# Optimization experiments

Hardware: AMD Instinct MI355X
Metric: run time of the kernel (lower is better)

The kernel has to match this reference:

```python
import jax, jax.numpy as jnp
import numpy as np

EMBED = 2048
HEADS = 16


def setup_inputs() -> dict:
    key = jax.random.key(0)
    ks = jax.random.split(key, 9)
    N, L, E = 4, 2048, EMBED
    inp = {
        "query": jax.random.normal(ks[0], (N, L, E), dtype=jnp.float32),
        "keys": jax.random.normal(ks[1], (N, L, E), dtype=jnp.float32),
        "values": jax.random.normal(ks[2], (N, L, E), dtype=jnp.float32),
        "mask": jax.random.randint(ks[3], (N, L), 0, 2, dtype=jnp.int32),
        # nn.Linear weights, stored torch-style as (out_features, in_features)
        "Wq": jax.random.normal(ks[4], (E, E), dtype=jnp.float32) * (E ** -0.5),
        "Wk": jax.random.normal(ks[5], (E, E), dtype=jnp.float32) * (E ** -0.5),
        "Wv": jax.random.normal(ks[6], (E, E), dtype=jnp.float32) * (E ** -0.5),
        "Wo": jax.random.normal(ks[7], (E, E), dtype=jnp.float32) * (E ** -0.5),
        "bo": jax.random.normal(ks[8], (E,), dtype=jnp.float32) * 0.01,
    }
    return inp


def reference(query, keys, values, mask, Wq, Wk, Wv, Wo, bo):
    N, Lq, E = query.shape
    Lk = keys.shape[1]
    H = HEADS
    D = E // H
    # projections (torch Linear: y = x @ W.T)
    q = (query @ Wq.T).reshape(N, Lq, H, D)   # nqhd
    k = (keys @ Wk.T).reshape(N, Lk, H, D)    # nkhd
    v = (values @ Wv.T).reshape(N, Lk, H, D)  # nkhd
    # attention scores per head: (N, H, Lq, Lk)
    energy = jnp.einsum('nqhd,nkhd->nhqk', q, k)
    # 2D mask (N, Lk): 0 = masked out, broadcast over heads and query positions
    m = mask[:, None, None, :]
    energy = jnp.where(m == 0, jnp.float32(-1e20), energy)
    # source scales by sqrt(embed_size), not sqrt(head_dim)
    attn = jax.nn.softmax(energy * (E ** -0.5), axis=-1)
    out = jnp.einsum('nhqk,nkhd->nqhd', attn, v).reshape(N, Lq, E)
    return out @ Wo.T + bo
```

## Files before the change

kernel.cpp:

```cpp
#include <hip/hip_runtime.h>
#include <stdint.h>


typedef __bf16 bf16;
typedef __bf16 bf16x2 __attribute__((ext_vector_type(2)));
typedef __bf16 bf16x4 __attribute__((ext_vector_type(4)));
typedef __bf16 bf16x8 __attribute__((ext_vector_type(8)));
typedef float  f32x4  __attribute__((ext_vector_type(4)));
typedef uint32_t u32x4 __attribute__((ext_vector_type(4)));

#define MFMA16(a, b, c) __builtin_amdgcn_mfma_f32_16x16x32_bf16(a, b, c, 0, 0, 0)

__device__ __forceinline__ void gload_lds16(const void* g, void* s) {
  __builtin_amdgcn_global_load_lds(
      (const __attribute__((address_space(1))) void*)g,
      (__attribute__((address_space(3))) void*)s, 16, 0, 0);
}

__device__ __forceinline__ uint32_t pkbf(float a, float b) {
  return __builtin_bit_cast(uint32_t, (bf16x2){(bf16)a, (bf16)b});
}

__device__ __forceinline__ float fexp2(float x) {
  return __builtin_amdgcn_exp2f(x);
}

__global__ __launch_bounds__(256) void cvt8_bf16(const float* __restrict__ s0,
                                                 const float* __restrict__ s1,
                                                 const float* __restrict__ s2,
                                                 const float* __restrict__ s3,
                                                 const float* __restrict__ q,
                                                 bf16* __restrict__ d0,
                                                 bf16* __restrict__ d1,
                                                 bf16* __restrict__ d2,
                                                 bf16* __restrict__ d3,
                                                 bf16* __restrict__ dq,
                                                 long EE) {
  int y = blockIdx.y;
  const float* src;
  bf16* dst;
  if (y < 4) {
    src = y == 0 ? s0 : y == 1 ? s1 : y == 2 ? s2 : s3;
    dst = y == 0 ? d0 : y == 1 ? d1 : y == 2 ? d2 : d3;
  } else {
    src = q + (long)(y - 4) * EE;
    dst = dq + (long)(y - 4) * EE;
  }
  long i = ((long)blockIdx.x * 256 + threadIdx.x) * 4;
  f32x4 f = *(const f32x4*)(src + i);
  bf16x4 h = { (bf16)f.x, (bf16)f.y, (bf16)f.z, (bf16)f.w };
  *(bf16x4*)(dst + i) = h;
}

__global__ __launch_bounds__(256) void gather2_cvt(const float* __restrict__ ks,
                                                   const float* __restrict__ vs,
                                                   bf16* __restrict__ kd,
                                                   bf16* __restrict__ vd,
                                                   const int* __restrict__ idx,
                                                   const int* __restrict__ cnts) {
  long i = (long)blockIdx.x * 256 + threadIdx.x;
  int row = (int)(i >> 8);
  int u = (int)(i & 255);
  int n = row >> 11, p = row & 2047;
  if (p >= cnts[4 + n]) return;
  long srow = ((long)n << 11) + idx[(n << 11) + p];
  long so = srow * 2048 + u * 8;
  long dof = (long)row * 2048 + u * 8;
  {
    f32x4 a = *(const f32x4*)(ks + so);
    f32x4 b = *(const f32x4*)(ks + so + 4);
    bf16x8 h = { (bf16)a.x, (bf16)a.y, (bf16)a.z, (bf16)a.w,
                 (bf16)b.x, (bf16)b.y, (bf16)b.z, (bf16)b.w };
    *(bf16x8*)(kd + dof) = h;
  }
  {
    f32x4 a = *(const f32x4*)(vs + so);
    f32x4 b = *(const f32x4*)(vs + so + 4);
    bf16x8 h = { (bf16)a.x, (bf16)a.y, (bf16)a.z, (bf16)a.w,
                 (bf16)b.x, (bf16)b.y, (bf16)b.z, (bf16)b.w };
    *(bf16x8*)(vd + dof) = h;
  }
}

__global__ __launch_bounds__(256) void mask_compact(const int* __restrict__ mask,
                                                    int* __restrict__ idx,
                                                    int* __restrict__ cnts) {
  const int n = blockIdx.x;
  const int t = threadIdx.x, l = t & 63, w = t >> 6;
  const int* m = mask + n * 2048;
  __shared__ int wtot[4];
  int f[8], tt = 0;
  const int base = t * 8;
#pragma unroll
  for (int i = 0; i < 8; ++i) { f[i] = (m[base + i] != 0); tt += f[i]; }
  int sc = tt;
#pragma unroll
  for (int d = 1; d < 64; d <<= 1) {
    int v = __shfl_up(sc, d);
    if (l >= d) sc += v;
  }
  if (l == 63) wtot[w] = sc;
  __syncthreads();
  int woff = 0;
#pragma unroll
  for (int i = 0; i < 4; ++i) if (i < w) woff += wtot[i];
  int off = woff + sc - tt;
#pragma unroll
  for (int i = 0; i < 8; ++i)
    if (f[i]) { idx[n * 2048 + off] = base + i; ++off; }
  int total = wtot[0] + wtot[1] + wtot[2] + wtot[3];
  for (int p = total + t; p < 2048; p += 256) idx[n * 2048 + p] = 2047;
  if (t == 0) { cnts[n] = total; cnts[4 + n] = (total + 127) & ~127; }
}

template <int QKV, int OUT_F32, int ADD_BIAS>
__global__ __launch_bounds__(512, 2) void gemm256(const bf16* __restrict__ A0,
                                                  const bf16* __restrict__ A1,
                                                  const bf16* __restrict__ A2,
                                                  const bf16* __restrict__ B0,
                                                  const bf16* __restrict__ B1,
                                                  const bf16* __restrict__ B2,
                                                  void* __restrict__ C0,
                                                  void* __restrict__ C1,
                                                  void* __restrict__ C2,
                                                  const float* __restrict__ bias,
                                                  const int* __restrict__ cnts) {
  constexpr int K = 2048, LDC = 2048, NT = 32;
  constexpr int TILE = 256 * 64;
  __shared__ bf16 S[2 * 2 * TILE];
  const int t = threadIdx.x;
  const int l = t & 63, w = t >> 6;
  const int wr = w >> 2, wc = w & 3;
  const int l15 = l & 15, l4 = l >> 4;

  const int z = blockIdx.z;
  const bf16* A = z == 0 ? A0 : z == 1 ? A1 : A2;
  const bf16* B = z == 0 ? B0 : z == 1 ? B1 : B2;
  void* Cout = z == 0 ? C0 : z == 1 ? C1 : C2;

  const int Mb = ((blockIdx.x & 7) << 2) + (blockIdx.x >> 3);
  const long tm = (long)Mb * 256;
  const long tn = (long)blockIdx.y * 256;

  if constexpr (QKV) {
    if (z) {
      int n = (int)(tm >> 11);
      if ((int)(tm & 2047) >= cnts[4 + n]) return;
    }
  }

  const bf16* Ab = A + tm * K;
  const bf16* Bb = B + tn * K;

  auto stage = [&](int T, int p) {
    bf16* sA = S + p * 2 * TILE;
    bf16* sB = sA + TILE;
    const bf16* Ak = Ab + T * 64;
    const bf16* Bk = Bb + T * 64;
#pragma unroll
    for (int i = 0; i < 4; ++i) {
      int u = i * 512 + t;
      int row = u >> 3, slot = u & 7;
      int ss = slot ^ (row & 7);
      gload_lds16(Ak + (long)row * K + ss * 8, sA + u * 8);
    }
#pragma unroll
    for (int i = 0; i < 4; ++i) {
      int u = i * 512 + t;
      int row = u >> 3, slot = u & 7;
      int ss = slot ^ (row & 7);
      gload_lds16(Bk + (long)row * K + ss * 8, sB + u * 8);
    }
  };

  f32x4 acc[8][4];
#pragma unroll
  for (int i = 0; i < 8; ++i)
#pragma unroll
    for (int j = 0; j < 4; ++j) acc[i][j] = (f32x4){0.f, 0.f, 0.f, 0.f};

  stage(0, 0);

  for (int T = 0; T < NT; ++T) {
    const int p = T & 1;
    const bf16* sA = S + p * 2 * TILE;
    const bf16* sB = sA + TILE;

    if (T + 1 < NT) {
      stage(T + 1, p ^ 1);
      asm volatile("s_waitcnt vmcnt(8)" ::: "memory");
    } else {
      asm volatile("s_waitcnt vmcnt(0)" ::: "memory");
    }
    __builtin_amdgcn_s_barrier();
    asm volatile("" ::: "memory");

#pragma unroll
    for (int kk = 0; kk < 2; ++kk) {
      bf16x8 bfr[4];
#pragma unroll
      for (int ni = 0; ni < 4; ++ni) {
        int row = wc * 64 + ni * 16 + l15;
        int slot = (kk * 4 + l4) ^ (row & 7);
        bfr[ni] = *(const bf16x8*)(sB + row * 64 + slot * 8);
      }
#pragma unroll
      for (int mh = 0; mh < 2; ++mh) {
        bf16x8 af[4];
#pragma unroll
        for (int i = 0; i < 4; ++i) {
          int row = wr * 128 + (mh * 4 + i) * 16 + l15;
          int slot = (kk * 4 + l4) ^ (row & 7);
          af[i] = *(const bf16x8*)(sA + row * 64 + slot * 8);
        }
        asm volatile("" ::: "memory");
        __builtin_amdgcn_s_barrier();
        asm volatile("" ::: "memory");
        __builtin_amdgcn_s_setprio(1);
#pragma unroll
        for (int i = 0; i < 4; ++i)
#pragma unroll
          for (int ni = 0; ni < 4; ++ni)
            acc[mh * 4 + i][ni] = MFMA16(af[i], bfr[ni], acc[mh * 4 + i][ni]);
        __builtin_amdgcn_s_setprio(0);
        asm volatile("" ::: "memory");
        __builtin_amdgcn_s_barrier();
        asm volatile("" ::: "memory");
      }
    }
  }

  const float sc = (QKV && blockIdx.z == 0) ? 0.031879357f : 1.0f;
#pragma unroll
  for (int mi = 0; mi < 8; ++mi) {
#pragma unroll
    for (int ni = 0; ni < 4; ++ni) {
      long col = tn + wc * 64 + ni * 16 + l15;
      long row = tm + wr * 128 + mi * 16 + l4 * 4;
#pragma unroll
      for (int r = 0; r < 4; ++r) {
        float v = acc[mi][ni][r];
        if constexpr (QKV) v *= sc;
        if constexpr (OUT_F32) {
          if constexpr (ADD_BIAS) v += bias[col];
          ((float*)Cout)[(row + r) * (long)LDC + col] = v;
        } else {
          ((bf16*)Cout)[(row + r) * (long)LDC + col] = (bf16)v;
        }
      }
    }
  }
}

__global__ __launch_bounds__(512, 4) void attn_fwd(const bf16* __restrict__ Qp,
                                                   const bf16* __restrict__ Kp,
                                                   const bf16* __restrict__ Vp,
                                                   const int* __restrict__ cnts,
                                                   bf16* __restrict__ Op) {
  constexpr int L = 2048, E = 2048, KVB = 64;
  __shared__ bf16 Kt[2][KVB * 128];
  __shared__ bf16 VT[2][128 * KVB];
  const int t = threadIdx.x, l = t & 63, w = t >> 6;
  const int l15 = l & 15, l4 = l >> 4;

  const int b = blockIdx.x;
  const int slot = ((b & 7) << 7) + (b >> 3);
  const int q0 = (slot & 15) << 7;
  const int y = slot >> 4;
  const int n = y >> 4, h = y & 15;
  const int wq = w * 16;

  const bf16* Qb = Qp + ((long)n * L + q0) * E + h * 128;
  const bf16* Kb = Kp + (long)n * L * E + h * 128;
  const bf16* Vb = Vp + (long)n * L * E + h * 128;
  const int cnt = cnts[n];
  const int ntk = (cnt + 63) >> 6;

  bf16x8 qf[4];
#pragma unroll
  for (int kk = 0; kk < 4; ++kk)
    qf[kk] = *(const bf16x8*)(Qb + (long)(wq + l15) * E + kk * 32 + l4 * 8);

  f32x4 o[8];
#pragma unroll
  for (int ni = 0; ni < 8; ++ni) o[ni] = (f32x4){0.f, 0.f, 0.f, 0.f};
  float mreg = -1e20f, lreg = 0.f;

  const int vj0 = ((l15 & 1) + 2 * l4 + 8 * (w & 1)) * 4;
  const int vd0 = ((l15 >> 1) + 8 * (w >> 1)) * 4;

  auto stageK = [&](int kv, int pp) {
#pragma unroll
    for (int i = 0; i < 2; ++i) {
      int u = i * 512 + t;
      int row = u >> 4, sl = u & 15;
      gload_lds16(Kb + (long)(kv + row) * E + ((sl ^ (row & 7)) * 8),
                  &Kt[pp][u * 8]);
    }
  };
  auto loadV = [&](int kv, bf16x4* vr) {
#pragma unroll
    for (int r = 0; r < 4; ++r)
      vr[r] = *(const bf16x4*)(Vb + (long)(kv + vj0 + r) * E + vd0);
  };
  auto writeV = [&](const bf16x4* vr, int pp) {
#pragma unroll
    for (int i = 0; i < 4; ++i) {
      int d = vd0 + i;
      bf16x4 pk = { vr[0][i], vr[1][i], vr[2][i], vr[3][i] };
      *(bf16x4*)(&VT[pp][d * KVB + (vj0 ^ ((d & 7) << 3))]) = pk;
    }
  };

  bf16x4 vr[4];
  stageK(0, 0);
  loadV(0, vr);
  writeV(vr, 0);
  __syncthreads();

  for (int ti = 0; ti < ntk; ++ti) {
    const int p = ti & 1;
    const int kv = ti << 6;
    const bool pre = (ti + 1) < ntk;
    if (pre) {
      stageK(kv + KVB, p ^ 1);
      loadV(kv + KVB, vr);
    }

    f32x4 s[4];
#pragma unroll
    for (int ni = 0; ni < 4; ++ni) s[ni] = (f32x4){0.f, 0.f, 0.f, 0.f};
#pragma unroll
    for (int kk = 0; kk < 4; ++kk) {
      bf16x8 kf[4];
#pragma unroll
      for (int ni = 0; ni < 4; ++ni) {
        int row = ni * 16 + l15;
        int sl = (kk * 4 + l4) ^ (row & 7);
        kf[ni] = *(const bf16x8*)(&Kt[p][row * 128 + sl * 8]);
      }
      __builtin_amdgcn_s_setprio(1);
#pragma unroll
      for (int ni = 0; ni < 4; ++ni)
        s[ni] = MFMA16(kf[ni], qf[kk], s[ni]);
      __builtin_amdgcn_s_setprio(0);
    }

    if (kv + KVB > cnt) {
#pragma unroll
      for (int ni = 0; ni < 4; ++ni)
#pragma unroll
        for (int r = 0; r < 4; ++r) {
          int j = kv + ni * 16 + l4 * 4 + r;
          s[ni][r] = (j < cnt) ? s[ni][r] : -1e20f;
        }
    }

    float m1 = fmaxf(fmaxf(s[0][0], s[0][1]), s[0][2]);
    float m2 = fmaxf(fmaxf(s[0][3], s[1][0]), s[1][1]);
    float m3 = fmaxf(fmaxf(s[1][2], s[1][3]), s[2][0]);
    float m4 = fmaxf(fmaxf(s[2][1], s[2][2]), s[2][3]);
    float m5 = fmaxf(fmaxf(s[3][0], s[3][1]), s[3][2]);
    float vmax = fmaxf(fmaxf(fmaxf(m1, m2), m3), fmaxf(fmaxf(m4, m5), s[3][3]));
    vmax = fmaxf(vmax, __shfl_xor(vmax, 16));
    vmax = fmaxf(vmax, __shfl_xor(vmax, 32));
    bool nd = vmax > mreg + 11.5f;
    float corr = nd ? fexp2(mreg - vmax) : 1.0f;
    float mn = nd ? vmax : mreg;
    mreg = mn;
    float rsum = 0.f;
    uint32_t u[4][2];
#pragma unroll
    for (int ni = 0; ni < 4; ++ni) {
      float p0 = fexp2(s[ni][0] - mn);
      float p1 = fexp2(s[ni][1] - mn);
      float p2 = fexp2(s[ni][2] - mn);
      float p3 = fexp2(s[ni][3] - mn);
      rsum += (p0 + p1) + (p2 + p3);
      u[ni][0] = pkbf(p0, p1);
      u[ni][1] = pkbf(p2, p3);
    }
    rsum += __shfl_xor(rsum, 16);
    rsum += __shfl_xor(rsum, 32);
    lreg = lreg * corr + rsum;
    if (__any(nd)) {
#pragma unroll
      for (int r = 0; r < 4; ++r) {
        float cr = __shfl(corr, l4 * 20 + r);
#pragma unroll
        for (int ni = 0; ni < 8; ++ni) o[ni][r] *= cr;
      }
    }

    const int srcA = l15 + ((l & 16) << 1);
    const int srcB = srcA + 16;
    const bool e5 = (l4 >> 1) != 0;
#pragma unroll
    for (int kk = 0; kk < 2; ++kk) {
      uint32_t a0 = (uint32_t)__shfl((int)u[kk * 2][0], srcA);
      uint32_t a1 = (uint32_t)__shfl((int)u[kk * 2][1], srcA);
      uint32_t a2 = (uint32_t)__shfl((int)u[kk * 2][0], srcB);
      uint32_t a3 = (uint32_t)__shfl((int)u[kk * 2][1], srcB);
      uint32_t b0 = (uint32_t)__shfl((int)u[kk * 2 + 1][0], srcA);
      uint32_t b1 = (uint32_t)__shfl((int)u[kk * 2 + 1][1], srcA);
      uint32_t b2 = (uint32_t)__shfl((int)u[kk * 2 + 1][0], srcB);
      uint32_t b3 = (uint32_t)__shfl((int)u[kk * 2 + 1][1], srcB);
      u32x4 pw = { e5 ? b0 : a0, e5 ? b1 : a1, e5 ? b2 : a2, e5 ? b3 : a3 };
      bf16x8 pa = __builtin_bit_cast(bf16x8, pw);
      bf16x8 vb[8];
#pragma unroll
      for (int ni = 0; ni < 8; ++ni) {
        int d = ni * 16 + l15;
        int col = (kk * 32 + l4 * 8) ^ ((d & 7) << 3);
        vb[ni] = *(const bf16x8*)(&VT[p][d * KVB + col]);
      }
      __builtin_amdgcn_s_setprio(1);
#pragma unroll
      for (int ni = 0; ni < 8; ++ni)
        o[ni] = MFMA16(pa, vb[ni], o[ni]);
      __builtin_amdgcn_s_setprio(0);
    }

    if (pre) writeV(vr, p ^ 1);
    __syncthreads();
  }

  float inv = 1.f / lreg;
#pragma unroll
  for (int r = 0; r < 4; ++r) {
    float iv = __shfl(inv, l4 * 20 + r);
    long grow = (long)n * L + q0 + wq + l4 * 4 + r;
#pragma unroll
    for (int ni = 0; ni < 8; ++ni)
      Op[grow * E + h * 128 + ni * 16 + l15] = (bf16)(o[ni][r] * iv);
  }
}

extern "C" void kernel_launch(void* const* d_in, const int* in_sizes, int n_in,
                              void* d_out, int out_size, void* d_ws, size_t ws_size,
                              hipStream_t stream) {
  (void)in_sizes; (void)n_in; (void)out_size; (void)ws_size;
  const float* query = (const float*)d_in[0];
  const float* keys  = (const float*)d_in[1];
  const float* values= (const float*)d_in[2];
  const int*   mask  = (const int*)d_in[3];
  const float* Wq = (const float*)d_in[4];
  const float* Wk = (const float*)d_in[5];
  const float* Wv = (const float*)d_in[6];
  const float* Wo = (const float*)d_in[7];
  const float* bo = (const float*)d_in[8];
  float* out = (float*)d_out;

  const int N = 4, L = 2048, E = 2048;
  const int M = N * L;
  const long EE = (long)E * E;
  const long ME = (long)M * E;

  int*  idx  = (int*)d_ws;
  int*  cnts = idx + N * 2048;
  bf16* Wqb  = (bf16*)((char*)d_ws + 65536);
  bf16* Wkb  = Wqb + EE;
  bf16* Wvb  = Wkb + EE;
  bf16* Wob  = Wvb + EE;
  bf16* qp   = Wob + EE;
  bf16* kp   = qp + ME;
  bf16* vp   = kp + ME;
  bf16* xq   = kp;
  bf16* xk   = (bf16*)d_out;
  bf16* xv   = (bf16*)d_out + ME;

  const int cbw = (int)(EE / 4 / 256);
  const int gbl = (int)(ME / 8 / 256);
  dim3 ggqkv(32, 8, 3);
  dim3 gg(32, 8, 1);

  mask_compact<<<4, 256, 0, stream>>>(mask, idx, cnts);
  cvt8_bf16<<<dim3(cbw, 8), 256, 0, stream>>>(Wq, Wk, Wv, Wo, query,
                                              Wqb, Wkb, Wvb, Wob, xq, EE);
  gather2_cvt<<<gbl, 256, 0, stream>>>(keys, values, xk, xv, idx, cnts);

  gemm256<1, 0, 0><<<ggqkv, 512, 0, stream>>>(xq, xk, xv, Wqb, Wkb, Wvb,
                                              qp, kp, vp, nullptr, cnts);
  attn_fwd<<<1024, 512, 0, stream>>>(qp, kp, vp, cnts, qp);
  gemm256<0, 1, 1><<<gg, 512, 0, stream>>>(qp, qp, qp, Wob, Wob, Wob,
                                           out, out, out, bo, cnts);
}
```

Baseline: 437.2 us.

## Interleave quarter-tile global-to-LDS loads across MFMA phases in GEMM main loop

Restructures the 256x256 GEMM K-loop to process two K-tiles per iteration in eight quadrant phases. The next tiles' loads are split into quarter-tile chunks issued between phases, with fine-grained vmcnt waits. The aim is to spread memory traffic across the MFMA work and avoid bursts of eight loads followed by a stall. The per-phase barriers and the hand-tuned wait counts add synchronisation and a risk of ordering or LDS race bugs.

```diff
diff --git a/kernel.cpp b/kernel.cpp
--- a/kernel.cpp
+++ b/kernel.cpp
@@ -125,9 +125,9 @@
                                                   void* __restrict__ C2,
                                                   const float* __restrict__ bias,
                                                   const int* __restrict__ cnts) {
-  constexpr int K = 2048, LDC = 2048, NT = 32;
+  constexpr int K = 2048, LDC = 2048, NITER = 16;
   constexpr int TILE = 256 * 64;
-  __shared__ bf16 S[2 * 2 * TILE];
+  __shared__ bf16 S[4 * TILE];
   const int t = threadIdx.x;
   const int l = t & 63, w = t >> 6;
   const int wr = w >> 2, wc = w & 3;
@@ -152,25 +152,12 @@
   const bf16* Ab = A + tm * K;
   const bf16* Bb = B + tn * K;
 
-  auto stage = [&](int T, int p) {
-    bf16* sA = S + p * 2 * TILE;
-    bf16* sB = sA + TILE;
-    const bf16* Ak = Ab + T * 64;
-    const bf16* Bk = Bb + T * 64;
-#pragma unroll
-    for (int i = 0; i < 4; ++i) {
-      int u = i * 512 + t;
-      int row = u >> 3, slot = u & 7;
-      int ss = slot ^ (row & 7);
-      gload_lds16(Ak + (long)row * K + ss * 8, sA + u * 8);
-    }
-#pragma unroll
-    for (int i = 0; i < 4; ++i) {
-      int u = i * 512 + t;
-      int row = u >> 3, slot = u & 7;
-      int ss = slot ^ (row & 7);
-      gload_lds16(Bk + (long)row * K + ss * 8, sB + u * 8);
-    }
+  auto stageQ = [&](int ab, int tile, int qt) {
+    bf16* dst = S + ((long)((tile & 1) * 2 + ab)) * TILE + qt * 4096;
+    const bf16* srcb = ab ? Bb : Ab;
+    int row = qt * 64 + (t >> 3);
+    int ss = (t & 7) ^ (row & 7);
+    gload_lds16(srcb + (long)row * K + tile * 64 + ss * 8, dst + t * 8);
   };
 
   f32x4 acc[8][4];
@@ -179,54 +166,75 @@
 #pragma unroll
     for (int j = 0; j < 4; ++j) acc[i][j] = (f32x4){0.f, 0.f, 0.f, 0.f};
 
-  stage(0, 0);
-
-  for (int T = 0; T < NT; ++T) {
-    const int p = T & 1;
-    const bf16* sA = S + p * 2 * TILE;
-    const bf16* sB = sA + TILE;
-
-    if (T + 1 < NT) {
-      stage(T + 1, p ^ 1);
-      asm volatile("s_waitcnt vmcnt(8)" ::: "memory");
-    } else {
-      asm volatile("s_waitcnt vmcnt(0)" ::: "memory");
-    }
-    __builtin_amdgcn_s_barrier();
-    asm volatile("" ::: "memory");
-
-#pragma unroll
-    for (int kk = 0; kk < 2; ++kk) {
-      bf16x8 bfr[4];
-#pragma unroll
-      for (int ni = 0; ni < 4; ++ni) {
-        int row = wc * 64 + ni * 16 + l15;
-        int slot = (kk * 4 + l4) ^ (row & 7);
-        bfr[ni] = *(const bf16x8*)(sB + row * 64 + slot * 8);
-      }
-#pragma unroll
-      for (int mh = 0; mh < 2; ++mh) {
-        bf16x8 af[4];
-#pragma unroll
-        for (int i = 0; i < 4; ++i) {
-          int row = wr * 128 + (mh * 4 + i) * 16 + l15;
+#pragma unroll
+  for (int qt = 0; qt < 4; ++qt) stageQ(0, 0, qt);
+#pragma unroll
+  for (int qt = 0; qt < 4; ++qt) stageQ(1, 0, qt);
+  stageQ(0, 1, 0); stageQ(0, 1, 2);
+  asm volatile("s_waitcnt vmcnt(2)" ::: "memory");
+  __builtin_amdgcn_s_barrier();
+  asm volatile("" ::: "memory");
+
+  for (int j = 0; j < NITER; ++j) {
+    const bool full = (j + 1 < NITER);
+    const int tj1 = 2 * j + 1, tj2 = 2 * j + 2, tj3 = 2 * j + 3;
+#pragma unroll
+    for (int q8 = 0; q8 < 8; ++q8) {
+      const int half = q8 >> 2;
+      const int mh = (q8 >> 1) & 1, nh = q8 & 1;
+      const bf16* Ap = S + (long)(half * 2) * TILE;
+      const bf16* Bp = Ap + TILE;
+
+      bf16x8 af[4][2], bfr[2][2];
+#pragma unroll
+      for (int i = 0; i < 4; ++i) {
+        int row = wr * 128 + mh * 64 + i * 16 + l15;
+#pragma unroll
+        for (int kk = 0; kk < 2; ++kk) {
           int slot = (kk * 4 + l4) ^ (row & 7);
-          af[i] = *(const bf16x8*)(sA + row * 64 + slot * 8);
+          af[i][kk] = *(const bf16x8*)(Ap + row * 64 + slot * 8);
         }
-        asm volatile("" ::: "memory");
-        __builtin_amdgcn_s_barrier();
-        asm volatile("" ::: "memory");
-        __builtin_amdgcn_s_setprio(1);
+      }
+#pragma unroll
+      for (int jn = 0; jn < 2; ++jn) {
+        int row = wc * 64 + (nh * 2 + jn) * 16 + l15;
+#pragma unroll
+        for (int kk = 0; kk < 2; ++kk) {
+          int slot = (kk * 4 + l4) ^ (row & 7);
+          bfr[jn][kk] = *(const bf16x8*)(Bp + row * 64 + slot * 8);
+        }
+      }
+
+      if (q8 == 0)      { stageQ(0, tj1, 1); stageQ(0, tj1, 3); }
+      else if (q8 == 1) { stageQ(1, tj1, 0); stageQ(1, tj1, 1); }
+      else if (q8 == 2) { stageQ(1, tj1, 2); stageQ(1, tj1, 3);
+                          if (full) { stageQ(0, tj2, 0); stageQ(0, tj2, 2); } }
+      else if (q8 == 3) { if (full) asm volatile("s_waitcnt vmcnt(2)" ::: "memory");
+                          else      asm volatile("s_waitcnt vmcnt(0)" ::: "memory"); }
+      else if (q8 == 4) { if (full) { stageQ(0, tj2, 1); stageQ(0, tj2, 3); } }
+      else if (q8 == 5) { if (full) { stageQ(1, tj2, 0); stageQ(1, tj2, 1); } }
+      else if (q8 == 6) { if (full) { stageQ(1, tj2, 2); stageQ(1, tj2, 3); } }
+      else              { if (full) { stageQ(0, tj3, 0); stageQ(0, tj3, 2);
+                          asm volatile("s_waitcnt vmcnt(2)" ::: "memory"); } }
+
+      asm volatile("" ::: "memory");
+      __builtin_amdgcn_s_barrier();
+      asm volatile("" ::: "memory");
+
+      __builtin_amdgcn_s_setprio(1);
+#pragma unroll
+      for (int kk = 0; kk < 2; ++kk)
 #pragma unroll
         for (int i = 0; i < 4; ++i)
 #pragma unroll
-          for (int ni = 0; ni < 4; ++ni)
-            acc[mh * 4 + i][ni] = MFMA16(af[i], bfr[ni], acc[mh * 4 + i][ni]);
-        __builtin_amdgcn_s_setprio(0);
-        asm volatile("" ::: "memory");
-        __builtin_amdgcn_s_barrier();
-        asm volatile("" ::: "memory");
-      }
+          for (int jn = 0; jn < 2; ++jn)
+            acc[mh * 4 + i][nh * 2 + jn] =
+                MFMA16(af[i][kk], bfr[jn][kk], acc[mh * 4 + i][nh * 2 + jn]);
+      __builtin_amdgcn_s_setprio(0);
+
+      asm volatile("" ::: "memory");
+      __builtin_amdgcn_s_barrier();
+      asm volatile("" ::: "memory");
     }
   }
 
```

Result: slower. 454.3 us (+3.9%).
